# Optimization experiments

Measured on AMD Instinct MI355X. Metric: run time of the kernel, lower is better.

Reference implementation:

```python
import jax, jax.numpy as jnp
import numpy as np

EPS = 1e-4  # Moller-Trumbore epsilon from the original

def _dot(a, b):
    return jnp.sum(a * b, axis=-1)

def setup_inputs() -> dict:
    key = jax.random.key(0)
    k1, k2, k3 = jax.random.split(key, 3)
    N, V, F = 2048, 2500, 4096
    p = jax.random.normal(k1, (N, 3), dtype=jnp.float32)
    v = jax.random.normal(k2, (V, 3), dtype=jnp.float32)
    f = jax.random.randint(k3, (F, 3), 0, V, dtype=jnp.int64)
    return {"p": p, "v": v, "f": f}

def reference(p, v, f):
    N = p.shape[0]
    faces = v[f]                      # (F,3,3)
    a, b, c = faces[:, 0], faces[:, 1], faces[:, 2]   # (F,3) each
    pe = p[None]                      # (1,N,3), broadcasts against (F,1,3)

    # --- point-to-triangle distance = min over the 3 edge segments (matches original output math) ---
    e1 = a - b                        # faces[:,0]-faces[:,1]
    e2 = c - b
    e3 = c - a

    def seg(e, ref_pt, q0, q1):
        # s = ((ref_pt - p) . e) / |e|^2, clamped; closest = s*q0 + (1-s)*q1  (original formula kept verbatim)
        m2 = _dot(e, e)[:, None]                       # (F,1)
        s = jnp.clip(_dot(ref_pt[:, None] - pe, e[:, None]) / m2, 0.0, 1.0)[..., None]  # (F,N,1)
        cl = s * q0[:, None] + (1.0 - s) * q1[:, None]  # (F,N,3)
        d = jnp.linalg.norm(cl - pe, axis=-1)           # (F,N)
        return d, cl

    d12, c12 = seg(e1, a, b, a)   # s12 from (p0-p).e1; closest = s*p1+(1-s)*p0
    d23, c23 = seg(e2, c, b, c)   # s23 from (p2-p).e2; closest = s*p1+(1-s)*p2
    d31, c31 = seg(e3, c, a, c)   # s31 from (p2-p).e3; closest = s*p0+(1-s)*p2

    d_all = jnp.stack([d12, d23, d31], axis=0)          # (3,F,N)
    c_all = jnp.stack([c12, c23, c31], axis=0)          # (3,F,N,3)
    which = jnp.argmin(d_all, axis=0)                   # (F,N)
    dist = jnp.min(d_all, axis=0)                       # (F,N)
    closest = jnp.take_along_axis(c_all, which[None, ..., None], axis=0)[0]  # (F,N,3)

    # nearest face per query point
    fidx = jnp.argmin(jnp.abs(dist), axis=0)            # (N,)
    dmin = jnp.take_along_axis(dist, fidx[None], axis=0)  # (1,N)
    closest_p = closest[fidx, jnp.arange(N)]            # (N,3)

    # --- Moller-Trumbore ray-triangle parity test toward mesh centroid ---
    dirv = v.mean(axis=0)[None] - p                     # (N,3)
    me1 = b - a                                         # faces[:,1]-faces[:,0]
    me2 = c - a
    pvec = jnp.cross(dirv[None], me2[:, None])          # (F,N,3)
    det = _dot(me1[:, None], pvec)                      # (F,N)
    tvec = pe - a[:, None]                              # (F,N,3)
    u = _dot(tvec, pvec) / det
    qvec = jnp.cross(tvec, me1[:, None])                # (F,N,3)
    dd = _dot(dirv[None], qvec) / det
    t = _dot(me2[:, None], qvec) / det
    hit = (jnp.abs(det) > EPS) & (u >= 0) & (u <= 1) & (dd >= 0) & (u + dd <= 1) & (t > EPS)
    counts = jnp.sum(hit, axis=0)                       # (N,)
    inside = (0.5 - (counts % 2 == 1).astype(dmin.dtype)) * 2.0  # +1 outside, -1 inside

    dmin = dmin * inside[None]                          # (1,N)
    return (dmin, closest_p)
```

## Files before the change

### kernel.cpp

```cpp
#include <hip/hip_runtime.h>
#include <math.h>

#define TRI_EPS 1e-4f

__global__ void vmean_kernel(const float* __restrict__ v, int V,
                             float* __restrict__ ws) {
    __shared__ float sx[256], sy[256], sz[256];
    int t = threadIdx.x;
    float x = 0.f, y = 0.f, z = 0.f;
    for (int i = t; i < V; i += 256) {
        x += v[3 * i + 0];
        y += v[3 * i + 1];
        z += v[3 * i + 2];
    }
    sx[t] = x; sy[t] = y; sz[t] = z;
    __syncthreads();
    for (int off = 128; off > 0; off >>= 1) {
        if (t < off) {
            sx[t] += sx[t + off];
            sy[t] += sy[t + off];
            sz[t] += sz[t + off];
        }
        __syncthreads();
    }
    if (t == 0) {
        ws[0] = sx[0] / (float)V;
        ws[1] = sy[0] / (float)V;
        ws[2] = sz[0] / (float)V;
    }
}

__global__ __launch_bounds__(256) void prep_kernel(
    const float* __restrict__ v, const int* __restrict__ f,
    float4* __restrict__ fd, int F) {
    int j = blockIdx.x * 256 + threadIdx.x;
    if (j >= F) return;
    const int i0 = f[3 * j + 0];
    const int i1 = f[3 * j + 1];
    const int i2 = f[3 * j + 2];
    const float ax = v[3 * i0 + 0], ay = v[3 * i0 + 1], az = v[3 * i0 + 2];
    const float bx = v[3 * i1 + 0], by = v[3 * i1 + 1], bz = v[3 * i1 + 2];
    const float cx = v[3 * i2 + 0], cy = v[3 * i2 + 1], cz = v[3 * i2 + 2];
    const float e1x = ax - bx, e1y = ay - by, e1z = az - bz;
    const float e2x = cx - bx, e2y = cy - by, e2z = cz - bz;
    const float e3x = cx - ax, e3y = cy - ay, e3z = cz - az;
    const float m1 = e1x * e1x + e1y * e1y + e1z * e1z;
    const float m2 = e2x * e2x + e2y * e2y + e2z * e2z;
    const float m3 = e3x * e3x + e3y * e3y + e3z * e3z;
    fd[3 * j + 0] = make_float4(ax, ay, az, 1.f / m1);
    fd[3 * j + 1] = make_float4(bx, by, bz, 1.f / m2);
    fd[3 * j + 2] = make_float4(cx, cy, cz, 1.f / m3);
}

__device__ __forceinline__ void pair_update(
    float ax, float ay, float az, float bx, float by, float bz,
    float cx, float cy, float cz, float inv1, float inv2, float inv3,
    float e1x, float e1y, float e1z, float e2x, float e2y, float e2z,
    float e3x, float e3y, float e3z,
    float px, float py, float pz, float dx, float dy, float dz, int j,
    float& bd2, int& bj, float& bcx, float& bcy, float& bcz, int& hits) {
    const float apx = ax - px, apy = ay - py, apz = az - pz;
    const float cpx = cx - px, cpy = cy - py, cpz = cz - pz;

    float s1 = (apx * e1x + apy * e1y + apz * e1z) * inv1;
    s1 = fminf(fmaxf(s1, 0.f), 1.f);
    const float o1 = 1.f - s1;
    const float x1 = s1 * bx + o1 * ax;
    const float y1 = s1 * by + o1 * ay;
    const float z1 = s1 * bz + o1 * az;
    float ux = x1 - px, uy = y1 - py, uz = z1 - pz;
    const float d1 = ux * ux + uy * uy + uz * uz;

    float s2 = (cpx * e2x + cpy * e2y + cpz * e2z) * inv2;
    s2 = fminf(fmaxf(s2, 0.f), 1.f);
    const float o2 = 1.f - s2;
    const float x2 = s2 * bx + o2 * cx;
    const float y2 = s2 * by + o2 * cy;
    const float z2 = s2 * bz + o2 * cz;
    ux = x2 - px; uy = y2 - py; uz = z2 - pz;
    const float d2 = ux * ux + uy * uy + uz * uz;

    float s3 = (cpx * e3x + cpy * e3y + cpz * e3z) * inv3;
    s3 = fminf(fmaxf(s3, 0.f), 1.f);
    const float o3 = 1.f - s3;
    const float x3 = s3 * ax + o3 * cx;
    const float y3 = s3 * ay + o3 * cy;
    const float z3 = s3 * az + o3 * cz;
    ux = x3 - px; uy = y3 - py; uz = z3 - pz;
    const float d3 = ux * ux + uy * uy + uz * uz;

    float fd2 = d1, fx = x1, fy = y1, fz = z1;
    if (d2 < fd2) { fd2 = d2; fx = x2; fy = y2; fz = z2; }
    if (d3 < fd2) { fd2 = d3; fx = x3; fy = y3; fz = z3; }
    if (fd2 < bd2) { bd2 = fd2; bj = j; bcx = fx; bcy = fy; bcz = fz; }

    const float pvx = dy * e3z - dz * e3y;
    const float pvy = dz * e3x - dx * e3z;
    const float pvz = dx * e3y - dy * e3x;
    const float det = -(e1x * pvx + e1y * pvy + e1z * pvz);
    const float tu = -(apx * pvx + apy * pvy + apz * pvz);
    const float qvx = apy * e1z - apz * e1y;
    const float qvy = apz * e1x - apx * e1z;
    const float qvz = apx * e1y - apy * e1x;
    const float td = dx * qvx + dy * qvy + dz * qvz;
    const float tn = e3x * qvx + e3y * qvy + e3z * qvz;
    const float adet = fabsf(det);
    const float sd = (det > 0.f) ? 1.f : -1.f;
    const float su = tu * sd;
    const float sq = td * sd;
    const float st = tn * sd;
    if (adet > TRI_EPS && su >= 0.f && su <= adet && sq >= 0.f &&
        (su + sq) <= adet && st > TRI_EPS * adet)
        hits++;
}

__global__ __launch_bounds__(256) void sdf_main(
    const float* __restrict__ p, const float4* __restrict__ fd,
    const float* __restrict__ vm, float* __restrict__ out, int N, int F) {
    const int t = threadIdx.x;
    const int i0 = blockIdx.x * 2;
    const int i1 = i0 + 1;
    const bool has1 = (i1 < N);

    const float vmx = vm[0], vmy = vm[1], vmz = vm[2];
    const float p0x = p[3 * i0 + 0], p0y = p[3 * i0 + 1], p0z = p[3 * i0 + 2];
    const float p1x = has1 ? p[3 * i1 + 0] : 0.f;
    const float p1y = has1 ? p[3 * i1 + 1] : 0.f;
    const float p1z = has1 ? p[3 * i1 + 2] : 0.f;
    const float d0x = vmx - p0x, d0y = vmy - p0y, d0z = vmz - p0z;
    const float d1x = vmx - p1x, d1y = vmy - p1y, d1z = vmz - p1z;

    float Abd2 = INFINITY; int Abj = 0x7fffffff;
    float Acx = 0.f, Acy = 0.f, Acz = 0.f; int Ah = 0;
    float Bbd2 = INFINITY; int Bbj = 0x7fffffff;
    float Bcx = 0.f, Bcy = 0.f, Bcz = 0.f; int Bh = 0;

    for (int j = t; j < F; j += 256) {
        const float4 ra = fd[3 * j + 0];
        const float4 rb = fd[3 * j + 1];
        const float4 rc = fd[3 * j + 2];
        const float ax = ra.x, ay = ra.y, az = ra.z, inv1 = ra.w;
        const float bx = rb.x, by = rb.y, bz = rb.z, inv2 = rb.w;
        const float cx = rc.x, cy = rc.y, cz = rc.z, inv3 = rc.w;
        const float e1x = ax - bx, e1y = ay - by, e1z = az - bz;
        const float e2x = cx - bx, e2y = cy - by, e2z = cz - bz;
        const float e3x = cx - ax, e3y = cy - ay, e3z = cz - az;

        pair_update(ax, ay, az, bx, by, bz, cx, cy, cz, inv1, inv2, inv3,
                    e1x, e1y, e1z, e2x, e2y, e2z, e3x, e3y, e3z,
                    p0x, p0y, p0z, d0x, d0y, d0z, j,
                    Abd2, Abj, Acx, Acy, Acz, Ah);
        pair_update(ax, ay, az, bx, by, bz, cx, cy, cz, inv1, inv2, inv3,
                    e1x, e1y, e1z, e2x, e2y, e2z, e3x, e3y, e3z,
                    p1x, p1y, p1z, d1x, d1y, d1z, j,
                    Bbd2, Bbj, Bcx, Bcy, Bcz, Bh);
    }

    __shared__ float sd2[2][256];
    __shared__ int sjj[2][256];
    __shared__ float scx[2][256], scy[2][256], scz[2][256];
    __shared__ int shh[2][256];
    sd2[0][t] = Abd2; sjj[0][t] = Abj;
    scx[0][t] = Acx; scy[0][t] = Acy; scz[0][t] = Acz; shh[0][t] = Ah;
    sd2[1][t] = Bbd2; sjj[1][t] = Bbj;
    scx[1][t] = Bcx; scy[1][t] = Bcy; scz[1][t] = Bcz; shh[1][t] = Bh;
    __syncthreads();
    for (int off = 128; off > 0; off >>= 1) {
        if (t < off) {
            #pragma unroll
            for (int q = 0; q < 2; q++) {
                const float dov = sd2[q][t + off];
                const int jov = sjj[q][t + off];
                if (dov < sd2[q][t] || (dov == sd2[q][t] && jov < sjj[q][t])) {
                    sd2[q][t] = dov; sjj[q][t] = jov;
                    scx[q][t] = scx[q][t + off];
                    scy[q][t] = scy[q][t + off];
                    scz[q][t] = scz[q][t + off];
                }
                shh[q][t] += shh[q][t + off];
            }
        }
        __syncthreads();
    }
    if (t == 0) {
        const float sg0 = (shh[0][0] & 1) ? -1.f : 1.f;
        out[i0] = sqrtf(sd2[0][0]) * sg0;
        out[N + 3 * i0 + 0] = scx[0][0];
        out[N + 3 * i0 + 1] = scy[0][0];
        out[N + 3 * i0 + 2] = scz[0][0];
        if (has1) {
            const float sg1 = (shh[1][0] & 1) ? -1.f : 1.f;
            out[i1] = sqrtf(sd2[1][0]) * sg1;
            out[N + 3 * i1 + 0] = scx[1][0];
            out[N + 3 * i1 + 1] = scy[1][0];
            out[N + 3 * i1 + 2] = scz[1][0];
        }
    }
}

extern "C" void kernel_launch(void* const* d_in, const int* in_sizes, int n_in,
                              void* d_out, int out_size, void* d_ws,
                              size_t ws_size, hipStream_t stream) {
    const float* p = (const float*)d_in[0];
    const float* v = (const float*)d_in[1];
    const int* f = (const int*)d_in[2];
    float* out = (float*)d_out;
    float* ws = (float*)d_ws;

    const int N = in_sizes[0] / 3;
    const int V = in_sizes[1] / 3;
    const int F = in_sizes[2] / 3;

    float4* fdat = (float4*)((char*)d_ws + 16);

    vmean_kernel<<<1, 256, 0, stream>>>(v, V, ws);
    prep_kernel<<<(F + 255) / 256, 256, 0, stream>>>(v, f, fdat, F);
    sdf_main<<<(N + 1) / 2, 256, 0, stream>>>(p, fdat, ws, out, N, F);
}
```

Before: 46.26 us.

## Fuse vertex-mean into prep, prefetch face data, recompute closest point at end

Merges the vertex-mean reduction into block 0 of the face-prep kernel, which removes one kernel launch. The main loop now software-prefetches the next face's data. Per-thread state becomes a packed face/edge id in place of the closest-point coordinates, which shrinks registers and shared-memory reduction traffic. Two threads then recompute the winning closest point at the end, at the cost of a small tail recompute and different tie-breaking encoding (face<<2|edge).

Measured after the change: 42.73 us. -7.6%, faster.

```diff
diff --git a/kernel.cpp b/kernel.cpp
--- a/kernel.cpp
+++ b/kernel.cpp
@@ -3,105 +3,125 @@
 
 #define TRI_EPS 1e-4f
 
-__global__ void vmean_kernel(const float* __restrict__ v, int V,
-                             float* __restrict__ ws) {
-    __shared__ float sx[256], sy[256], sz[256];
-    int t = threadIdx.x;
-    float x = 0.f, y = 0.f, z = 0.f;
-    for (int i = t; i < V; i += 256) {
-        x += v[3 * i + 0];
-        y += v[3 * i + 1];
-        z += v[3 * i + 2];
-    }
-    sx[t] = x; sy[t] = y; sz[t] = z;
-    __syncthreads();
-    for (int off = 128; off > 0; off >>= 1) {
-        if (t < off) {
-            sx[t] += sx[t + off];
-            sy[t] += sy[t + off];
-            sz[t] += sz[t + off];
-        }
-        __syncthreads();
-    }
-    if (t == 0) {
-        ws[0] = sx[0] / (float)V;
-        ws[1] = sy[0] / (float)V;
-        ws[2] = sz[0] / (float)V;
-    }
-}
-
 __global__ __launch_bounds__(256) void prep_kernel(
     const float* __restrict__ v, const int* __restrict__ f,
-    float4* __restrict__ fd, int F) {
-    int j = blockIdx.x * 256 + threadIdx.x;
-    if (j >= F) return;
-    const int i0 = f[3 * j + 0];
-    const int i1 = f[3 * j + 1];
-    const int i2 = f[3 * j + 2];
-    const float ax = v[3 * i0 + 0], ay = v[3 * i0 + 1], az = v[3 * i0 + 2];
-    const float bx = v[3 * i1 + 0], by = v[3 * i1 + 1], bz = v[3 * i1 + 2];
-    const float cx = v[3 * i2 + 0], cy = v[3 * i2 + 1], cz = v[3 * i2 + 2];
-    const float e1x = ax - bx, e1y = ay - by, e1z = az - bz;
-    const float e2x = cx - bx, e2y = cy - by, e2z = cz - bz;
-    const float e3x = cx - ax, e3y = cy - ay, e3z = cz - az;
-    const float m1 = e1x * e1x + e1y * e1y + e1z * e1z;
-    const float m2 = e2x * e2x + e2y * e2y + e2z * e2z;
-    const float m3 = e3x * e3x + e3y * e3y + e3z * e3z;
-    fd[3 * j + 0] = make_float4(ax, ay, az, 1.f / m1);
-    fd[3 * j + 1] = make_float4(bx, by, bz, 1.f / m2);
-    fd[3 * j + 2] = make_float4(cx, cy, cz, 1.f / m3);
-}
-
-__device__ __forceinline__ void pair_update(
-    float ax, float ay, float az, float bx, float by, float bz,
-    float cx, float cy, float cz, float inv1, float inv2, float inv3,
-    float e1x, float e1y, float e1z, float e2x, float e2y, float e2z,
-    float e3x, float e3y, float e3z,
-    float px, float py, float pz, float dx, float dy, float dz, int j,
-    float& bd2, int& bj, float& bcx, float& bcy, float& bcz, int& hits) {
-    const float apx = ax - px, apy = ay - py, apz = az - pz;
+    float4* __restrict__ fdat, float* __restrict__ vm, int V, int F) {
+    const int t = threadIdx.x;
+    const int j = blockIdx.x * 256 + t;
+    if (j < F) {
+        const int i0 = f[3 * j + 0];
+        const int i1 = f[3 * j + 1];
+        const int i2 = f[3 * j + 2];
+        const float ax = v[3 * i0 + 0], ay = v[3 * i0 + 1], az = v[3 * i0 + 2];
+        const float bx = v[3 * i1 + 0], by = v[3 * i1 + 1], bz = v[3 * i1 + 2];
+        const float cx = v[3 * i2 + 0], cy = v[3 * i2 + 1], cz = v[3 * i2 + 2];
+        const float e1x = ax - bx, e1y = ay - by, e1z = az - bz;
+        const float e2x = cx - bx, e2y = cy - by, e2z = cz - bz;
+        const float e3x = cx - ax, e3y = cy - ay, e3z = cz - az;
+        const float m1 = e1x * e1x + e1y * e1y + e1z * e1z;
+        const float m2 = e2x * e2x + e2y * e2y + e2z * e2z;
+        const float m3 = e3x * e3x + e3y * e3y + e3z * e3z;
+        fdat[3 * j + 0] = make_float4(ax, ay, az, 1.f / m1);
+        fdat[3 * j + 1] = make_float4(bx, by, bz, 1.f / m2);
+        fdat[3 * j + 2] = make_float4(cx, cy, cz, 1.f / m3);
+    }
+    if (blockIdx.x == 0) {
+        __shared__ float sx[256], sy[256], sz[256];
+        float x = 0.f, y = 0.f, z = 0.f;
+        for (int i = t; i < V; i += 256) {
+            x += v[3 * i + 0];
+            y += v[3 * i + 1];
+            z += v[3 * i + 2];
+        }
+        sx[t] = x; sy[t] = y; sz[t] = z;
+        __syncthreads();
+        for (int off = 128; off > 0; off >>= 1) {
+            if (t < off) {
+                sx[t] += sx[t + off];
+                sy[t] += sy[t + off];
+                sz[t] += sz[t + off];
+            }
+            __syncthreads();
+        }
+        if (t == 0) {
+            vm[0] = sx[0] / (float)V;
+            vm[1] = sy[0] / (float)V;
+            vm[2] = sz[0] / (float)V;
+        }
+    }
+}
+
+struct FP {
+    float d1, d2, d3;
+    float x1, y1, z1, x2, y2, z2, x3, y3, z3;
+    float apx, apy, apz;
+};
+
+__device__ __forceinline__ FP face_point(
+    const float4 ra, const float4 rb, const float4 rc,
+    const float e1x, const float e1y, const float e1z,
+    const float e2x, const float e2y, const float e2z,
+    const float e3x, const float e3y, const float e3z,
+    const float px, const float py, const float pz) {
+    FP r;
+    const float ax = ra.x, ay = ra.y, az = ra.z;
+    const float bx = rb.x, by = rb.y, bz = rb.z;
+    const float cx = rc.x, cy = rc.y, cz = rc.z;
+    r.apx = ax - px; r.apy = ay - py; r.apz = az - pz;
     const float cpx = cx - px, cpy = cy - py, cpz = cz - pz;
 
-    float s1 = (apx * e1x + apy * e1y + apz * e1z) * inv1;
+    float s1 = (r.apx * e1x + r.apy * e1y + r.apz * e1z) * ra.w;
     s1 = fminf(fmaxf(s1, 0.f), 1.f);
     const float o1 = 1.f - s1;
-    const float x1 = s1 * bx + o1 * ax;
-    const float y1 = s1 * by + o1 * ay;
-    const float z1 = s1 * bz + o1 * az;
-    float ux = x1 - px, uy = y1 - py, uz = z1 - pz;
-    const float d1 = ux * ux + uy * uy + uz * uz;
-
-    float s2 = (cpx * e2x + cpy * e2y + cpz * e2z) * inv2;
+    r.x1 = s1 * bx + o1 * ax;
+    r.y1 = s1 * by + o1 * ay;
+    r.z1 = s1 * bz + o1 * az;
+    float ux = r.x1 - px, uy = r.y1 - py, uz = r.z1 - pz;
+    r.d1 = ux * ux + uy * uy + uz * uz;
+
+    float s2 = (cpx * e2x + cpy * e2y + cpz * e2z) * rb.w;
     s2 = fminf(fmaxf(s2, 0.f), 1.f);
     const float o2 = 1.f - s2;
-    const float x2 = s2 * bx + o2 * cx;
-    const float y2 = s2 * by + o2 * cy;
-    const float z2 = s2 * bz + o2 * cz;
-    ux = x2 - px; uy = y2 - py; uz = z2 - pz;
-    const float d2 = ux * ux + uy * uy + uz * uz;
-
-    float s3 = (cpx * e3x + cpy * e3y + cpz * e3z) * inv3;
+    r.x2 = s2 * bx + o2 * cx;
+    r.y2 = s2 * by + o2 * cy;
+    r.z2 = s2 * bz + o2 * cz;
+    ux = r.x2 - px; uy = r.y2 - py; uz = r.z2 - pz;
+    r.d2 = ux * ux + uy * uy + uz * uz;
+
+    float s3 = (cpx * e3x + cpy * e3y + cpz * e3z) * rc.w;
     s3 = fminf(fmaxf(s3, 0.f), 1.f);
     const float o3 = 1.f - s3;
-    const float x3 = s3 * ax + o3 * cx;
-    const float y3 = s3 * ay + o3 * cy;
-    const float z3 = s3 * az + o3 * cz;
-    ux = x3 - px; uy = y3 - py; uz = z3 - pz;
-    const float d3 = ux * ux + uy * uy + uz * uz;
-
-    float fd2 = d1, fx = x1, fy = y1, fz = z1;
-    if (d2 < fd2) { fd2 = d2; fx = x2; fy = y2; fz = z2; }
-    if (d3 < fd2) { fd2 = d3; fx = x3; fy = y3; fz = z3; }
-    if (fd2 < bd2) { bd2 = fd2; bj = j; bcx = fx; bcy = fy; bcz = fz; }
+    r.x3 = s3 * ax + o3 * cx;
+    r.y3 = s3 * ay + o3 * cy;
+    r.z3 = s3 * az + o3 * cz;
+    ux = r.x3 - px; uy = r.y3 - py; uz = r.z3 - pz;
+    r.d3 = ux * ux + uy * uy + uz * uz;
+    return r;
+}
+
+__device__ __forceinline__ void pair_update(
+    const float4 ra, const float4 rb, const float4 rc,
+    const float e1x, const float e1y, const float e1z,
+    const float e2x, const float e2y, const float e2z,
+    const float e3x, const float e3y, const float e3z,
+    const float px, const float py, const float pz,
+    const float dx, const float dy, const float dz, const int j,
+    float& bd2, int& bid, int& hits) {
+    const FP r = face_point(ra, rb, rc, e1x, e1y, e1z, e2x, e2y, e2z,
+                            e3x, e3y, e3z, px, py, pz);
+    float fd2 = r.d1; int eid = 0;
+    if (r.d2 < fd2) { fd2 = r.d2; eid = 1; }
+    if (r.d3 < fd2) { fd2 = r.d3; eid = 2; }
+    if (fd2 < bd2) { bd2 = fd2; bid = (j << 2) | eid; }
 
     const float pvx = dy * e3z - dz * e3y;
     const float pvy = dz * e3x - dx * e3z;
     const float pvz = dx * e3y - dy * e3x;
     const float det = -(e1x * pvx + e1y * pvy + e1z * pvz);
-    const float tu = -(apx * pvx + apy * pvy + apz * pvz);
-    const float qvx = apy * e1z - apz * e1y;
-    const float qvy = apz * e1x - apx * e1z;
-    const float qvz = apx * e1y - apy * e1x;
+    const float tu = -(r.apx * pvx + r.apy * pvy + r.apz * pvz);
+    const float qvx = r.apy * e1z - r.apz * e1y;
+    const float qvy = r.apz * e1x - r.apx * e1z;
+    const float qvz = r.apx * e1y - r.apy * e1x;
     const float td = dx * qvx + dy * qvy + dz * qvz;
     const float tn = e3x * qvx + e3y * qvy + e3z * qvz;
     const float adet = fabsf(det);
@@ -130,70 +150,86 @@
     const float d0x = vmx - p0x, d0y = vmy - p0y, d0z = vmz - p0z;
     const float d1x = vmx - p1x, d1y = vmy - p1y, d1z = vmz - p1z;
 
-    float Abd2 = INFINITY; int Abj = 0x7fffffff;
-    float Acx = 0.f, Acy = 0.f, Acz = 0.f; int Ah = 0;
-    float Bbd2 = INFINITY; int Bbj = 0x7fffffff;
-    float Bcx = 0.f, Bcy = 0.f, Bcz = 0.f; int Bh = 0;
-
-    for (int j = t; j < F; j += 256) {
-        const float4 ra = fd[3 * j + 0];
-        const float4 rb = fd[3 * j + 1];
-        const float4 rc = fd[3 * j + 2];
-        const float ax = ra.x, ay = ra.y, az = ra.z, inv1 = ra.w;
-        const float bx = rb.x, by = rb.y, bz = rb.z, inv2 = rb.w;
-        const float cx = rc.x, cy = rc.y, cz = rc.z, inv3 = rc.w;
-        const float e1x = ax - bx, e1y = ay - by, e1z = az - bz;
-        const float e2x = cx - bx, e2y = cy - by, e2z = cz - bz;
-        const float e3x = cx - ax, e3y = cy - ay, e3z = cz - az;
-
-        pair_update(ax, ay, az, bx, by, bz, cx, cy, cz, inv1, inv2, inv3,
-                    e1x, e1y, e1z, e2x, e2y, e2z, e3x, e3y, e3z,
-                    p0x, p0y, p0z, d0x, d0y, d0z, j,
-                    Abd2, Abj, Acx, Acy, Acz, Ah);
-        pair_update(ax, ay, az, bx, by, bz, cx, cy, cz, inv1, inv2, inv3,
-                    e1x, e1y, e1z, e2x, e2y, e2z, e3x, e3y, e3z,
-                    p1x, p1y, p1z, d1x, d1y, d1z, j,
-                    Bbd2, Bbj, Bcx, Bcy, Bcz, Bh);
+    float Ad2 = INFINITY; int Aid = 0x7fffffff; int Ah = 0;
+    float Bd2 = INFINITY; int Bid = 0x7fffffff; int Bh = 0;
+
+    int j = t;
+    bool valid = (j < F);
+    float4 ra, rb, rc;
+    if (valid) {
+        ra = fd[3 * j + 0];
+        rb = fd[3 * j + 1];
+        rc = fd[3 * j + 2];
+    }
+    while (valid) {
+        const int jn = j + 256;
+        const bool vn = (jn < F);
+        float4 na, nb, nc;
+        if (vn) {
+            na = fd[3 * jn + 0];
+            nb = fd[3 * jn + 1];
+            nc = fd[3 * jn + 2];
+        }
+        const float e1x = ra.x - rb.x, e1y = ra.y - rb.y, e1z = ra.z - rb.z;
+        const float e2x = rc.x - rb.x, e2y = rc.y - rb.y, e2z = rc.z - rb.z;
+        const float e3x = rc.x - ra.x, e3y = rc.y - ra.y, e3z = rc.z - ra.z;
+
+        pair_update(ra, rb, rc, e1x, e1y, e1z, e2x, e2y, e2z, e3x, e3y, e3z,
+                    p0x, p0y, p0z, d0x, d0y, d0z, j, Ad2, Aid, Ah);
+        pair_update(ra, rb, rc, e1x, e1y, e1z, e2x, e2y, e2z, e3x, e3y, e3z,
+                    p1x, p1y, p1z, d1x, d1y, d1z, j, Bd2, Bid, Bh);
+
+        j = jn; valid = vn;
+        ra = na; rb = nb; rc = nc;
     }
 
     __shared__ float sd2[2][256];
-    __shared__ int sjj[2][256];
-    __shared__ float scx[2][256], scy[2][256], scz[2][256];
+    __shared__ int sid[2][256];
     __shared__ int shh[2][256];
-    sd2[0][t] = Abd2; sjj[0][t] = Abj;
-    scx[0][t] = Acx; scy[0][t] = Acy; scz[0][t] = Acz; shh[0][t] = Ah;
-    sd2[1][t] = Bbd2; sjj[1][t] = Bbj;
-    scx[1][t] = Bcx; scy[1][t] = Bcy; scz[1][t] = Bcz; shh[1][t] = Bh;
+    sd2[0][t] = Ad2; sid[0][t] = Aid; shh[0][t] = Ah;
+    sd2[1][t] = Bd2; sid[1][t] = Bid; shh[1][t] = Bh;
     __syncthreads();
     for (int off = 128; off > 0; off >>= 1) {
         if (t < off) {
             #pragma unroll
             for (int q = 0; q < 2; q++) {
                 const float dov = sd2[q][t + off];
-                const int jov = sjj[q][t + off];
-                if (dov < sd2[q][t] || (dov == sd2[q][t] && jov < sjj[q][t])) {
-                    sd2[q][t] = dov; sjj[q][t] = jov;
-                    scx[q][t] = scx[q][t + off];
-                    scy[q][t] = scy[q][t + off];
-                    scz[q][t] = scz[q][t + off];
+                const int iov = sid[q][t + off];
+                if (dov < sd2[q][t] || (dov == sd2[q][t] && iov < sid[q][t])) {
+                    sd2[q][t] = dov;
+                    sid[q][t] = iov;
                 }
                 shh[q][t] += shh[q][t + off];
             }
         }
         __syncthreads();
     }
-    if (t == 0) {
-        const float sg0 = (shh[0][0] & 1) ? -1.f : 1.f;
-        out[i0] = sqrtf(sd2[0][0]) * sg0;
-        out[N + 3 * i0 + 0] = scx[0][0];
-        out[N + 3 * i0 + 1] = scy[0][0];
-        out[N + 3 * i0 + 2] = scz[0][0];
-        if (has1) {
-            const float sg1 = (shh[1][0] & 1) ? -1.f : 1.f;
-            out[i1] = sqrtf(sd2[1][0]) * sg1;
-            out[N + 3 * i1 + 0] = scx[1][0];
-            out[N + 3 * i1 + 1] = scy[1][0];
-            out[N + 3 * i1 + 2] = scz[1][0];
+
+    if (t < 2) {
+        const int i = i0 + t;
+        if (i < N) {
+            const float px = t ? p1x : p0x;
+            const float py = t ? p1y : p0y;
+            const float pz = t ? p1z : p0z;
+            const int bid = sid[t][0];
+            const int jw = bid >> 2;
+            const int eid = bid & 3;
+            const float4 wa = fd[3 * jw + 0];
+            const float4 wb = fd[3 * jw + 1];
+            const float4 wc = fd[3 * jw + 2];
+            const float e1x = wa.x - wb.x, e1y = wa.y - wb.y, e1z = wa.z - wb.z;
+            const float e2x = wc.x - wb.x, e2y = wc.y - wb.y, e2z = wc.z - wb.z;
+            const float e3x = wc.x - wa.x, e3y = wc.y - wa.y, e3z = wc.z - wa.z;
+            const FP r = face_point(wa, wb, wc, e1x, e1y, e1z, e2x, e2y, e2z,
+                                    e3x, e3y, e3z, px, py, pz);
+            float clx = r.x1, cly = r.y1, clz = r.z1;
+            if (eid == 1) { clx = r.x2; cly = r.y2; clz = r.z2; }
+            if (eid == 2) { clx = r.x3; cly = r.y3; clz = r.z3; }
+            const float d = sqrtf(sd2[t][0]);
+            out[i] = (shh[t][0] & 1) ? -d : d;
+            out[N + 3 * i + 0] = clx;
+            out[N + 3 * i + 1] = cly;
+            out[N + 3 * i + 2] = clz;
         }
     }
 }
@@ -213,7 +249,6 @@
 
     float4* fdat = (float4*)((char*)d_ws + 16);
 
-    vmean_kernel<<<1, 256, 0, stream>>>(v, V, ws);
-    prep_kernel<<<(F + 255) / 256, 256, 0, stream>>>(v, f, fdat, F);
+    prep_kernel<<<(F + 255) / 256, 256, 0, stream>>>(v, f, fdat, ws, V, F);
     sdf_main<<<(N + 1) / 2, 256, 0, stream>>>(p, fdat, ws, out, N, F);
 }
```
